# Performance work log

Measured on AMD Instinct MI355X. Metric: run time of the kernel, lower is better.

Reference implementation:

```python
import jax, jax.numpy as jnp
import numpy as np

B, T, D, H = 8, 2048, 1024, 64


def setup_inputs() -> dict:
    key = jax.random.key(0)
    k1, k2, k3, k4 = jax.random.split(key, 4)
    scale = 1.0 / np.sqrt(D)
    return {
        "x": jax.random.normal(k1, (B, T, D), dtype=jnp.float32),
        "Wq": jax.random.normal(k2, (D, H), dtype=jnp.float32) * scale,
        "Wk": jax.random.normal(k3, (D, H), dtype=jnp.float32) * scale,
        "Wv": jax.random.normal(k4, (D, H), dtype=jnp.float32) * scale,
    }


def reference(x, Wq, Wk, Wv):
    # x: [B, T, D]; projections to [B, T, H]
    q = jnp.einsum("btd,dh->bth", x, Wq)
    k = jnp.einsum("btd,dh->bth", x, Wk)
    v = jnp.einsum("btd,dh->bth", x, Wv)
    head_size = k.shape[-1]
    # scores: [B, T, T], scaled by head_size**-0.5
    wei = jnp.einsum("bqh,bkh->bqk", q, k) * (head_size ** -0.5)
    t = q.shape[1]
    causal = jnp.tril(jnp.ones((t, t), dtype=bool))  # [T, T]
    wei = jnp.where(causal, wei, -jnp.inf)
    wei = jax.nn.softmax(wei, axis=-1)
    # dropout p=0.0 (eval) -> identity
    out = jnp.einsum("bqk,bkh->bqh", wei, v)  # [B, T, H]
    return out
```

## Files before the change

### kernel.cpp

```cpp
#include <hip/hip_runtime.h>
#include <hip/hip_bf16.h>

typedef __attribute__((ext_vector_type(8))) __bf16 bf16x8;
typedef __attribute__((ext_vector_type(4))) float f32x4;

namespace {
constexpr int kB = 8;
constexpr int kT = 2048;
constexpr int kD = 1024;
constexpr int kH = 64;
}

__global__ __launch_bounds__(256) void wt_kernel(
    const float* __restrict__ Wq, const float* __restrict__ Wk,
    const float* __restrict__ Wv, __bf16* __restrict__ wtf) {
  const int wid = threadIdx.x >> 6;
  const int lane = threadIdx.x & 63;
  const int lr = lane & 15;
  const int lg = lane >> 4;
  const int p = blockIdx.x * 4 + wid;
  const int nt = p >> 5;
  const int ks = p & 31;
  const float* W = (nt < 4) ? Wq : ((nt < 8) ? Wk : Wv);
  const float scale = (nt < 4) ? 0.18033688011112042f : 1.0f;
  const int col = (nt & 3) * 16 + lr;
  bf16x8 v;
#pragma unroll
  for (int j = 0; j < 8; ++j)
    v[j] = (__bf16)(W[(size_t)(ks * 32 + lg * 8 + j) * kH + col] * scale);
  *(bf16x8*)(wtf + (size_t)p * 512 + lane * 8) = v;
}

__global__ __launch_bounds__(256, 2) void proj_kernel(
    const float* __restrict__ x, const __bf16* __restrict__ wtf,
    __bf16* __restrict__ Q, __bf16* __restrict__ K, __bf16* __restrict__ vf) {
  __shared__ alignas(16) char lds_raw[65536];
  float* p_s = (float*)lds_raw;

  const int tid = threadIdx.x;
  const int wid = tid >> 6;
  const int lane = tid & 63;
  const int lr = lane & 15;
  const int lg = lane >> 4;
  const int row0 = blockIdx.x * 32;

#pragma unroll
  for (int i = 0; i < 16; ++i) {
    const int c = i * 256 + tid;
    const int row = c >> 7;
    const int kc = c & 127;
    const float* src = x + (size_t)(row0 + row) * kD + kc * 8;
    const float4 a = ((const float4*)src)[0];
    const float4 b = ((const float4*)src)[1];
    bf16x8 v;
    v[0] = (__bf16)a.x; v[1] = (__bf16)a.y; v[2] = (__bf16)a.z; v[3] = (__bf16)a.w;
    v[4] = (__bf16)b.x; v[5] = (__bf16)b.y; v[6] = (__bf16)b.z; v[7] = (__bf16)b.w;
    const int byte = row * 2048 + ((kc * 16) ^ ((row & 7) << 4));
    *(bf16x8*)(lds_raw + byte) = v;
  }
  __syncthreads();

  f32x4 acc[2][12];
#pragma unroll
  for (int a = 0; a < 2; ++a)
#pragma unroll
    for (int nt = 0; nt < 12; ++nt) acc[a][nt] = (f32x4)(0.0f);

  const int swz = (lr & 7) << 4;
#pragma unroll 2
  for (int i = 0; i < 8; ++i) {
    const int kb = (wid * 256 + i * 32 + lg * 8) * 2;
    const bf16x8 a0 = *(const bf16x8*)(lds_raw + lr * 2048 + (kb ^ swz));
    const bf16x8 a1 = *(const bf16x8*)(lds_raw + 32768 + lr * 2048 + (kb ^ swz));
#pragma unroll
    for (int nt = 0; nt < 12; ++nt) {
      const bf16x8 bfrag =
          *(const bf16x8*)(wtf + (size_t)(nt * 32 + wid * 8 + i) * 512 + lane * 8);
      acc[0][nt] = __builtin_amdgcn_mfma_f32_16x16x32_bf16(a0, bfrag, acc[0][nt], 0, 0, 0);
      acc[1][nt] = __builtin_amdgcn_mfma_f32_16x16x32_bf16(a1, bfrag, acc[1][nt], 0, 0, 0);
    }
  }

  const int col = tid & 15;
  const int rowq = tid >> 4;
#pragma unroll
  for (int p = 0; p < 2; ++p) {
    __syncthreads();
#pragma unroll
    for (int j = 0; j < 12; ++j)
      *(f32x4*)&p_s[((wid * 12 + j) * 64 + lane) * 4] = acc[p][j];
    __syncthreads();
    const size_t g = (size_t)row0 + p * 16 + rowq;
    const int b = (int)(g >> 11);
    const int t = (int)(g & 2047);
#pragma unroll
    for (int j = 0; j < 12; ++j) {
      const int base = ((j * 64 + (rowq >> 2) * 16 + col) << 2) | (rowq & 3);
      const float v =
          p_s[base] + p_s[base + 3072] + p_s[base + 6144] + p_s[base + 9216];
      if (j < 4) {
        Q[g * kH + j * 16 + col] = (__bf16)v;
      } else if (j < 8) {
        K[g * kH + (j - 4) * 16 + col] = (__bf16)v;
      } else {
        vf[(((size_t)b * 64 + (t >> 5)) * 4 + (j - 8)) * 512 +
           ((t & 31) >> 3) * 128 + col * 8 + (t & 7)] = (__bf16)v;
      }
    }
  }
}

__global__ __launch_bounds__(256, 4) void attn_kernel(
    const __bf16* __restrict__ Q, const __bf16* __restrict__ K,
    const __bf16* __restrict__ vf, float* __restrict__ out) {
  __shared__ alignas(16) float o_s[4][16][68];
  __shared__ float m_s[4][16], l_s[4][16];

  const int wid = threadIdx.x >> 6;
  const int lane = threadIdx.x & 63;
  const int lr = lane & 15;
  const int lg = lane >> 4;
  const int b = blockIdx.y;
  const int qt = (int)gridDim.x - 1 - (int)blockIdx.x;
  const int q0 = qt * 16;

  const __bf16* Qb = Q + (size_t)b * kT * kH;
  const __bf16* Kb = K + (size_t)b * kT * kH;
  const __bf16* Vb = vf + (size_t)b * kH * kT;

  const bf16x8 aq0 = *(const bf16x8*)(Qb + (size_t)(q0 + lr) * kH + lg * 8);
  const bf16x8 aq1 = *(const bf16x8*)(Qb + (size_t)(q0 + lr) * kH + 32 + lg * 8);

  f32x4 o[4];
#pragma unroll
  for (int i = 0; i < 4; ++i) o[i] = (f32x4)(0.0f);
  float m = -1e30f, l = 0.0f;

  const int ntiles = (q0 + 16 + 31) >> 5;
  const int krow = 8 * (lr >> 2) + (lr & 3);

  for (int t = wid; t < ntiles; t += 4) {
    const int kv = t * 32;
    const __bf16* kp0 = Kb + (size_t)(kv + krow) * kH + lg * 8;
    const __bf16* kp1 = kp0 + (size_t)4 * kH;

    f32x4 s0 = (f32x4)(0.0f), s1 = (f32x4)(0.0f);
    s0 = __builtin_amdgcn_mfma_f32_16x16x32_bf16(
        *(const bf16x8*)(kp0), aq0, s0, 0, 0, 0);
    s0 = __builtin_amdgcn_mfma_f32_16x16x32_bf16(
        *(const bf16x8*)(kp0 + 32), aq1, s0, 0, 0, 0);
    s1 = __builtin_amdgcn_mfma_f32_16x16x32_bf16(
        *(const bf16x8*)(kp1), aq0, s1, 0, 0, 0);
    s1 = __builtin_amdgcn_mfma_f32_16x16x32_bf16(
        *(const bf16x8*)(kp1 + 32), aq1, s1, 0, 0, 0);

    if (kv + 31 > q0) {
      const int q = q0 + lr;
#pragma unroll
      for (int r = 0; r < 4; ++r) {
        if (kv + 8 * lg + r > q) s0[r] = -1e30f;
        if (kv + 8 * lg + 4 + r > q) s1[r] = -1e30f;
      }
    }

    float pm = fmaxf(fmaxf(fmaxf(s0[0], s0[1]), fmaxf(s0[2], s0[3])),
                     fmaxf(fmaxf(s1[0], s1[1]), fmaxf(s1[2], s1[3])));
    pm = fmaxf(pm, __shfl_xor(pm, 16, 64));
    pm = fmaxf(pm, __shfl_xor(pm, 32, 64));
    const float mn = fmaxf(m, pm);
    const float alpha = exp2f(m - mn);
    m = mn;

    float p0[4], p1[4];
    float sum = 0.0f;
#pragma unroll
    for (int r = 0; r < 4; ++r) {
      p0[r] = exp2f(s0[r] - mn);
      p1[r] = exp2f(s1[r] - mn);
      sum += p0[r] + p1[r];
    }
    sum += __shfl_xor(sum, 16, 64);
    sum += __shfl_xor(sum, 32, 64);
    l = l * alpha + sum;

    bf16x8 pb;
#pragma unroll
    for (int r = 0; r < 4; ++r) {
      pb[r] = (__bf16)p0[r];
      pb[r + 4] = (__bf16)p1[r];
    }

#pragma unroll
    for (int ht = 0; ht < 4; ++ht) {
      o[ht] = o[ht] * alpha;
      const bf16x8 va =
          *(const bf16x8*)(Vb + ((size_t)(kv >> 5) * 4 + ht) * 512 + lane * 8);
      o[ht] = __builtin_amdgcn_mfma_f32_16x16x32_bf16(va, pb, o[ht], 0, 0, 0);
    }
  }

#pragma unroll
  for (int ht = 0; ht < 4; ++ht)
    *(f32x4*)&o_s[wid][lr][ht * 16 + lg * 4] = o[ht];
  if (lg == 0) {
    m_s[wid][lr] = m;
    l_s[wid][lr] = l;
  }
  __syncthreads();

  const int ti = threadIdx.x;
  const int q = ti & 15;
  const int hb = ti >> 4;
  float mm = fmaxf(fmaxf(m_s[0][q], m_s[1][q]), fmaxf(m_s[2][q], m_s[3][q]));
  f32x4 acc = (f32x4)(0.0f);
  float ll = 0.0f;
#pragma unroll
  for (int w = 0; w < 4; ++w) {
    const float sc = exp2f(m_s[w][q] - mm);
    ll += sc * l_s[w][q];
    const f32x4 ov = *(const f32x4*)&o_s[w][q][hb * 4];
    acc += ov * sc;
  }
  const float inv = 1.0f / ll;
  *(f32x4*)(out + ((size_t)b * kT + q0 + q) * kH + hb * 4) = acc * inv;
}

extern "C" void kernel_launch(void* const* d_in, const int* in_sizes, int n_in,
                              void* d_out, int out_size, void* d_ws, size_t ws_size,
                              hipStream_t stream) {
  (void)in_sizes; (void)n_in; (void)out_size; (void)ws_size;
  const float* x  = (const float*)d_in[0];
  const float* Wq = (const float*)d_in[1];
  const float* Wk = (const float*)d_in[2];
  const float* Wv = (const float*)d_in[3];
  float* out = (float*)d_out;

  char* ws = (char*)d_ws;
  __bf16* wtf = (__bf16*)(ws);
  __bf16* Qp  = (__bf16*)(ws + 393216);
  __bf16* Kp  = (__bf16*)(ws + 393216 + 2097152);
  __bf16* vf  = (__bf16*)(ws + 393216 + 2 * 2097152);

  wt_kernel<<<96, 256, 0, stream>>>(Wq, Wk, Wv, wtf);
  proj_kernel<<<kB * kT / 32, 256, 0, stream>>>(x, wtf, Qp, Kp, vf);
  attn_kernel<<<dim3(kT / 16, kB), 256, 0, stream>>>(Qp, Kp, vf, out);
}
```

Before: 150.5 us.

## Pre-swizzle K into MFMA fragment layout and prefetch next K/V tile

The projection kernel now writes K in a fragment-major layout, so each lane reads one contiguous 16-byte chunk per MFMA operand, matching the existing V layout. The attention kernel register double-buffers K and V fragments, loading the tile for iteration t+4 while computing on the current tile. This aims to hide global-load latency in the serial online-softmax loop and to make the K reads fully coalesced. In exchange it raises register pressure under the 4-blocks-per-CU launch bound and adds a redundant load on the last iteration.

```diff
diff --git a/kernel.cpp b/kernel.cpp
--- a/kernel.cpp
+++ b/kernel.cpp
@@ -33,7 +33,7 @@
 
 __global__ __launch_bounds__(256, 2) void proj_kernel(
     const float* __restrict__ x, const __bf16* __restrict__ wtf,
-    __bf16* __restrict__ Q, __bf16* __restrict__ K, __bf16* __restrict__ vf) {
+    __bf16* __restrict__ Q, __bf16* __restrict__ kf, __bf16* __restrict__ vf) {
   __shared__ alignas(16) char lds_raw[65536];
   float* p_s = (float*)lds_raw;
 
@@ -101,7 +101,15 @@
       if (j < 4) {
         Q[g * kH + j * 16 + col] = (__bf16)v;
       } else if (j < 8) {
-        K[g * kH + (j - 4) * 16 + col] = (__bf16)v;
+        const int h = (j - 4) * 16 + col;
+        const int r = t & 31;
+        const int lrk = ((r >> 3) << 2) | (r & 3);
+        const int sub = (r >> 2) & 1;
+        const int dh = h >> 5;
+        const int lgk = (h & 31) >> 3;
+        const int jj = h & 7;
+        kf[(((size_t)b * 64 + (t >> 5)) * 4 + sub * 2 + dh) * 512 +
+           (lgk * 16 + lrk) * 8 + jj] = (__bf16)v;
       } else {
         vf[(((size_t)b * 64 + (t >> 5)) * 4 + (j - 8)) * 512 +
            ((t & 31) >> 3) * 128 + col * 8 + (t & 7)] = (__bf16)v;
@@ -111,7 +119,7 @@
 }
 
 __global__ __launch_bounds__(256, 4) void attn_kernel(
-    const __bf16* __restrict__ Q, const __bf16* __restrict__ K,
+    const __bf16* __restrict__ Q, const __bf16* __restrict__ kf,
     const __bf16* __restrict__ vf, float* __restrict__ out) {
   __shared__ alignas(16) float o_s[4][16][68];
   __shared__ float m_s[4][16], l_s[4][16];
@@ -125,8 +133,8 @@
   const int q0 = qt * 16;
 
   const __bf16* Qb = Q + (size_t)b * kT * kH;
-  const __bf16* Kb = K + (size_t)b * kT * kH;
-  const __bf16* Vb = vf + (size_t)b * kH * kT;
+  const __bf16* Kf = kf + (size_t)b * 131072 + lane * 8;
+  const __bf16* Vf = vf + (size_t)b * 131072 + lane * 8;
 
   const bf16x8 aq0 = *(const bf16x8*)(Qb + (size_t)(q0 + lr) * kH + lg * 8);
   const bf16x8 aq1 = *(const bf16x8*)(Qb + (size_t)(q0 + lr) * kH + 32 + lg * 8);
@@ -137,22 +145,32 @@
   float m = -1e30f, l = 0.0f;
 
   const int ntiles = (q0 + 16 + 31) >> 5;
-  const int krow = 8 * (lr >> 2) + (lr & 3);
+
+  bf16x8 ka[4], va[4];
+  {
+    const int t0c = (wid < ntiles) ? wid : 0;
+#pragma unroll
+    for (int c = 0; c < 4; ++c) {
+      ka[c] = *(const bf16x8*)(Kf + ((size_t)t0c * 4 + c) * 512);
+      va[c] = *(const bf16x8*)(Vf + ((size_t)t0c * 4 + c) * 512);
+    }
+  }
 
   for (int t = wid; t < ntiles; t += 4) {
+    const int tn = (t + 4 < ntiles) ? (t + 4) : t;
+    bf16x8 kn[4], vn[4];
+#pragma unroll
+    for (int c = 0; c < 4; ++c) {
+      kn[c] = *(const bf16x8*)(Kf + ((size_t)tn * 4 + c) * 512);
+      vn[c] = *(const bf16x8*)(Vf + ((size_t)tn * 4 + c) * 512);
+    }
+
     const int kv = t * 32;
-    const __bf16* kp0 = Kb + (size_t)(kv + krow) * kH + lg * 8;
-    const __bf16* kp1 = kp0 + (size_t)4 * kH;
-
     f32x4 s0 = (f32x4)(0.0f), s1 = (f32x4)(0.0f);
-    s0 = __builtin_amdgcn_mfma_f32_16x16x32_bf16(
-        *(const bf16x8*)(kp0), aq0, s0, 0, 0, 0);
-    s0 = __builtin_amdgcn_mfma_f32_16x16x32_bf16(
-        *(const bf16x8*)(kp0 + 32), aq1, s0, 0, 0, 0);
-    s1 = __builtin_amdgcn_mfma_f32_16x16x32_bf16(
-        *(const bf16x8*)(kp1), aq0, s1, 0, 0, 0);
-    s1 = __builtin_amdgcn_mfma_f32_16x16x32_bf16(
-        *(const bf16x8*)(kp1 + 32), aq1, s1, 0, 0, 0);
+    s0 = __builtin_amdgcn_mfma_f32_16x16x32_bf16(ka[0], aq0, s0, 0, 0, 0);
+    s0 = __builtin_amdgcn_mfma_f32_16x16x32_bf16(ka[1], aq1, s0, 0, 0, 0);
+    s1 = __builtin_amdgcn_mfma_f32_16x16x32_bf16(ka[2], aq0, s1, 0, 0, 0);
+    s1 = __builtin_amdgcn_mfma_f32_16x16x32_bf16(ka[3], aq1, s1, 0, 0, 0);
 
     if (kv + 31 > q0) {
       const int q = q0 + lr;
@@ -193,9 +211,13 @@
 #pragma unroll
     for (int ht = 0; ht < 4; ++ht) {
       o[ht] = o[ht] * alpha;
-      const bf16x8 va =
-          *(const bf16x8*)(Vb + ((size_t)(kv >> 5) * 4 + ht) * 512 + lane * 8);
-      o[ht] = __builtin_amdgcn_mfma_f32_16x16x32_bf16(va, pb, o[ht], 0, 0, 0);
+      o[ht] = __builtin_amdgcn_mfma_f32_16x16x32_bf16(va[ht], pb, o[ht], 0, 0, 0);
+    }
+
+#pragma unroll
+    for (int c = 0; c < 4; ++c) {
+      ka[c] = kn[c];
+      va[c] = vn[c];
     }
   }
 
@@ -238,10 +260,10 @@
   char* ws = (char*)d_ws;
   __bf16* wtf = (__bf16*)(ws);
   __bf16* Qp  = (__bf16*)(ws + 393216);
-  __bf16* Kp  = (__bf16*)(ws + 393216 + 2097152);
-  __bf16* vf  = (__bf16*)(ws + 393216 + 2 * 2097152);
+  __bf16* kfp = (__bf16*)(ws + 393216 + 2097152);
+  __bf16* vfp = (__bf16*)(ws + 393216 + 2 * 2097152);
 
   wt_kernel<<<96, 256, 0, stream>>>(Wq, Wk, Wv, wtf);
-  proj_kernel<<<kB * kT / 32, 256, 0, stream>>>(x, wtf, Qp, Kp, vf);
-  attn_kernel<<<dim3(kT / 16, kB), 256, 0, stream>>>(Qp, Kp, vf, out);
-}
+  proj_kernel<<<kB * kT / 32, 256, 0, stream>>>(x, wtf, Qp, kfp, vfp);
+  attn_kernel<<<dim3(kT / 16, kB), 256, 0, stream>>>(Qp, kfp, vfp, out);
+}
```

Result: faster. 135.1 us (-10.2%).
